# Kernel optimization log

Hardware: AMD Instinct MI355X
Metric: run time of the kernel (lower is better)

The kernel has to match this reference:

```python
import jax, jax.numpy as jnp
import numpy as np

K = 16        # neighbors (init kwarg k)
LN_EPS = 1e-5


def setup_inputs() -> dict:
    key = jax.random.key(0)
    ks = jax.random.split(key, 12)
    B, N, C, H = 4, 4096, 64, 12
    w = lambda k, s: jax.random.normal(k, s, jnp.float32) * 0.05
    d = {}
    d["x"] = jax.random.normal(ks[0], (B, N, C), jnp.float32)
    d["pos"] = jax.random.uniform(ks[1], (B, N, 3), jnp.float32)
    # to_q / to_k / to_v (bias=False). Stored as [in,out]; apply as x @ W.
    d["Wq"] = w(ks[2], (C, C)); d["Wk"] = w(ks[3], (C, C)); d["Wv"] = w(ks[4], (C, C))
    # pos_mlp: Linear(3,H) -> LayerNorm(H) -> ReLU -> Linear(H,C)
    d["p_w1"] = w(ks[5], (3, H)); d["p_b1"] = jnp.zeros((H,), jnp.float32)
    d["p_g"] = jnp.ones((H,), jnp.float32); d["p_be"] = jnp.zeros((H,), jnp.float32)
    d["p_w2"] = w(ks[6], (H, C)); d["p_b2"] = jnp.zeros((C,), jnp.float32)
    # attn_mlp: Linear(C,C) -> LayerNorm(C) -> ReLU -> Linear(C,C)
    d["a_w1"] = w(ks[7], (C, C)); d["a_b1"] = jnp.zeros((C,), jnp.float32)
    d["a_g"] = jnp.ones((C,), jnp.float32); d["a_be"] = jnp.zeros((C,), jnp.float32)
    d["a_w2"] = w(ks[8], (C, C)); d["a_b2"] = jnp.zeros((C,), jnp.float32)
    return d


def _ln(x, g, b):
    m = x.mean(-1, keepdims=True)
    v = ((x - m) ** 2).mean(-1, keepdims=True)
    return (x - m) * jax.lax.rsqrt(v + LN_EPS) * g + b


def _gather(feats, idx):
    # feats [B,N,C], idx [B,N,K] -> [B,N,K,C]
    return jax.vmap(lambda f, i: f[i])(feats, idx)


def reference(x, pos, Wq, Wk, Wv, p_w1, p_b1, p_g, p_be, p_w2, p_b2,
              a_w1, a_b1, a_g, a_be, a_w2, a_b2):
    # knn_points(pos, pos, K, return_sorted=True): K nearest by squared dist
    sq = jnp.sum(pos * pos, axis=-1)                       # [B,N]
    d2 = sq[:, :, None] + sq[:, None, :] - 2.0 * jnp.einsum('bnd,bmd->bnm', pos, pos)
    _, idx = jax.lax.top_k(-d2, K)                         # [B,N,K], ascending distance
    knn_xyz = _gather(pos, idx)                            # [B,N,K,3]
    q = x @ Wq                                             # [B,N,C]
    k = _gather(x @ Wk, idx)                               # [B,N,K,C]
    v = _gather(x @ Wv, idx)                               # [B,N,K,C]
    rel = pos[:, :, None, :] - knn_xyz                     # [B,N,K,3]
    pos_enc = jax.nn.relu(_ln(rel @ p_w1 + p_b1, p_g, p_be)) @ p_w2 + p_b2   # [B,N,K,C]
    w_in = q[:, :, None, :] - k + pos_enc                  # [B,N,K,C]
    attn = jax.nn.relu(_ln(w_in @ a_w1 + a_b1, a_g, a_be)) @ a_w2 + a_b2
    attn = jax.nn.softmax(attn, axis=-2)                   # softmax over K neighbors
    return jnp.einsum('bikd,bikd->bid', attn, v + pos_enc) # [B,N,C]
```

## Files before the change

kernel.cpp:

```cpp
#include <hip/hip_runtime.h>
#include <math.h>

#define NPTS 4096
#define KNN 16
#define LN_EPS 1e-5f

#define BOOT 128
#define CAP0 32
#define TRIG 24
#define CAP1 72
#define C1S  928
#define CHSZ 1056
#define SEG  352


__global__ __launch_bounds__(256) void proj3_kernel(
    const float* __restrict__ x, const float* __restrict__ Wq,
    const float* __restrict__ Wk, const float* __restrict__ Wv,
    float* __restrict__ qf, float* __restrict__ kf, float* __restrict__ vf) {
  int g = blockIdx.x * 256 + threadIdx.x;
  int r = g >> 6, c = g & 63;
  float sq = 0.f, sk = 0.f, sv = 0.f;
  for (int i = 0; i < 64; ++i) {
    float xv = x[r*64 + i];
    sq += xv * Wq[i*64 + c];
    sk += xv * Wk[i*64 + c];
    sv += xv * Wv[i*64 + c];
  }
  qf[g] = sq; kf[g] = sk; vf[g] = sv;
}

__global__ __launch_bounds__(256) void wtrans_kernel(
    const float* __restrict__ a_w1, const float* __restrict__ a_w2,
    float* __restrict__ w1t, float* __restrict__ w2t) {
  int e = blockIdx.x * 256 + threadIdx.x;
  int i = e >> 6, c = e & 63;
  w1t[c*64 + i] = a_w1[e];
  w2t[c*64 + i] = a_w2[e];
}

#define INSERT_CHAIN(DD, JJ)                                          \
  do {                                                                \
    float dd = (DD); int jj = (JJ);                                   \
    _Pragma("unroll")                                                 \
    for (int v = 0; v < 16; ++v) {                                    \
      bool sw = dd < ld[v];                                           \
      float nd = sw ? dd : ld[v]; float td = sw ? ld[v] : dd;         \
      int   nj = sw ? jj : lj[v]; int   tj = sw ? lj[v] : jj;         \
      ld[v] = nd; lj[v] = nj; dd = td; jj = tj;                       \
    }                                                                 \
  } while (0)

#define REPLAY0()                                                     \
  do {                                                                \
    for (int i = 0; ; ++i) {                                          \
      unsigned long long alive = __ballot(i < cnt);                   \
      if (!alive) break;                                              \
      if (i < cnt) {                                                  \
        float dd0 = s_buf0[i*128 + bo];                               \
        int   jj0 = __float_as_int(s_buf0[i*128 + bo + 1]);           \
        if (dd0 < ld[15]) INSERT_CHAIN(dd0, jj0);                     \
      }                                                               \
    }                                                                 \
    cnt = 0; thr = ld[15]; s_thr[tid] = thr;                          \
  } while (0)

#define GROUP_D2(SBASE)                                               \
  float4 p[8];                                                        \
  _Pragma("unroll")                                                   \
  for (int u = 0; u < 8; ++u) p[u] = s_p[(SBASE) + u];                \
  float d2v[8];                                                       \
  _Pragma("unroll")                                                   \
  for (int u = 0; u < 8; ++u) {                                       \
    float acc = __fmul_rn(qx, p[u].x);                                \
    acc = __fmaf_rn(qy, p[u].y, acc);                                 \
    acc = __fmaf_rn(qz, p[u].z, acc);                                 \
    d2v[u] = __fsub_rn(__fadd_rn(sqn, p[u].w), __fmul_rn(2.0f, acc)); \
  }

#define TREE_OFFS(THRV)                                               \
  int f0 = (d2v[0] < (THRV)) ? 1 : 0, f1 = (d2v[1] < (THRV)) ? 1 : 0, \
      f2 = (d2v[2] < (THRV)) ? 1 : 0, f3 = (d2v[3] < (THRV)) ? 1 : 0, \
      f4 = (d2v[4] < (THRV)) ? 1 : 0, f5 = (d2v[5] < (THRV)) ? 1 : 0, \
      f6 = (d2v[6] < (THRV)) ? 1 : 0, f7 = (d2v[7] < (THRV)) ? 1 : 0; \
  int s01 = f0+f1, s23 = f2+f3, s45 = f4+f5, s67 = f6+f7;             \
  int s03 = s01+s23, s47 = s45+s67;                                   \
  int o[8];                                                           \
  o[0] = cnt;        o[1] = cnt + f0;   o[2] = cnt + s01;             \
  o[3] = cnt + s01 + f2;                o[4] = cnt + s03;             \
  o[5] = o[4] + f4;  o[6] = o[4] + s45; o[7] = o[6] + f6;

__global__ __launch_bounds__(256) void knn_gated4_kernel(
    const float* __restrict__ pos, int* __restrict__ idx_out) {
  __shared__ __align__(16) float4 s_p[NPTS];
  __shared__ __align__(16) float  s_buf0[CAP0*128];
  __shared__ int   s_j1[3][(CAP1+1)*64];
  __shared__ float s_thr[64];
  __shared__ int   s_cnt1[3][64];
  __shared__ int   s_gen;
  __shared__ int   s_ovf;

  int t = threadIdx.x;
  int tid = t & 63, w = t >> 6, b = blockIdx.y;
  const float* pb = pos + b*NPTS*3;
  for (int j = t; j < NPTS; j += 256) {
    float px = pb[j*3+0], py = pb[j*3+1], pz = pb[j*3+2];
    float sq = __fadd_rn(__fadd_rn(__fmul_rn(px,px), __fmul_rn(py,py)),
                         __fmul_rn(pz,pz));
    s_p[j] = make_float4(px, py, pz, sq);
  }
  if (t < 64) s_thr[t] = INFINITY;
  if (t == 0) { s_ovf = 0; s_gen = 0; }
  __syncthreads();

  int n = blockIdx.x * 64 + tid;
  float4 qp = s_p[n];
  float qx = qp.x, qy = qp.y, qz = qp.z, sqn = qp.w;
  float ld[16]; int lj[16];
#pragma unroll
  for (int u = 0; u < 16; ++u) { ld[u] = INFINITY; lj[u] = 0x7fffffff; }

  for (int s = 0; s < BOOT; s += 8) {
    GROUP_D2(s)
#pragma unroll
    for (int u = 0; u < 8; ++u) {
      float d2 = d2v[u];
      if (d2 < ld[15]) INSERT_CHAIN(d2, s + u);
    }
  }
  float thr = ld[15];
  int bo = tid << 1;
  int cnt = 0;

  if (w == 0) {
    for (int s = BOOT; s < C1S; s += 8) {
      GROUP_D2(s)
      TREE_OFFS(thr)
#pragma unroll
      for (int u = 0; u < 8; ++u) {
        s_buf0[o[u]*128 + bo]     = d2v[u];
        s_buf0[o[u]*128 + bo + 1] = __int_as_float(s + u);
      }
      cnt += s03 + s47;
      int done = s + 8;
      bool pub = ((done & 127) == 0) && done >= 256 && done <= 896;
      if (pub || __ballot(cnt >= TRIG) != 0ULL) {
        REPLAY0();
        if (pub) {
          __threadfence_block();
          s_gen = (done >> 7) - 1;
        }
      }
    }
    REPLAY0();
    __syncthreads();

    int ovf = s_ovf;
    for (int ch = 0; ch < 3; ++ch) {
      int cs = C1S + ch*CHSZ;
      if (ovf & (1 << ch)) {
        int ce = cs + CHSZ;
        for (int s = cs; s < ce; s += 8) {
          GROUP_D2(s)
          TREE_OFFS(thr)
#pragma unroll
          for (int u = 0; u < 8; ++u) {
            s_buf0[o[u]*128 + bo]     = d2v[u];
            s_buf0[o[u]*128 + bo + 1] = __int_as_float(s + u);
          }
          cnt += s03 + s47;
          if (__ballot(cnt >= TRIG) != 0ULL) REPLAY0();
        }
        REPLAY0();
      } else {
        const int* jb = &s_j1[ch][0];
        int cc = s_cnt1[ch][tid];
        int jn = (0 < cc) ? jb[tid] : 0;
        float4 pn = s_p[jn];
        for (int i = 0; ; ++i) {
          unsigned long long alive = __ballot(i < cc);
          if (!alive) break;
          int jj0 = jn; float4 pj = pn;
          int ix = i + 1;
          jn = (ix < cc) ? jb[ix*64 + tid] : 0;
          pn = s_p[jn];
          if (i < cc) {
            float acc = __fmul_rn(qx, pj.x);
            acc = __fmaf_rn(qy, pj.y, acc);
            acc = __fmaf_rn(qz, pj.z, acc);
            float dd0 = __fsub_rn(__fadd_rn(sqn, pj.w), __fmul_rn(2.0f, acc));
            if (dd0 < ld[15]) INSERT_CHAIN(dd0, jj0);
          }
        }
      }
    }
    int* outp = idx_out + (b*NPTS + n)*KNN;
#pragma unroll
    for (int u = 0; u < 16; ++u) outp[u] = b*NPTS + lj[u];
  } else {
    int cs = C1S + (w-1)*CHSZ;
    int* jb = &s_j1[w-1][0];
    float thrW = thr;
#pragma unroll
    for (int seg = 0; seg < 3; ++seg) {
      int need = 2*seg + 2;
      while (*((volatile int*)&s_gen) < need) __builtin_amdgcn_s_sleep(2);
      thrW = fminf(thrW, *((volatile float*)&s_thr[tid]));
      int ss = cs + seg*SEG, se = ss + SEG;
      for (int s = ss; s < se; s += 8) {
        GROUP_D2(s)
        TREE_OFFS(thrW)
#pragma unroll
        for (int u = 0; u < 8; ++u) {
          int oc = (o[u] <= CAP1) ? o[u] : CAP1;
          jb[oc*64 + tid] = s + u;
        }
        cnt += s03 + s47;
      }
    }
    s_cnt1[w-1][tid] = (cnt <= CAP1) ? cnt : CAP1;
    if (cnt > CAP1) atomicOr(&s_ovf, 1 << (w-1));
    __syncthreads();
  }
}

__device__ __forceinline__ float wsum64(float v) {
  v += __shfl_xor(v, 1);
  v += __shfl_xor(v, 2);
  v += __shfl_xor(v, 4);
  v += __shfl_xor(v, 8);
  v += __shfl_xor(v, 16);
  v += __shfl_xor(v, 32);
  return v;
}

__device__ __forceinline__ float bcast(float v, int lane) {
  return __int_as_float(__builtin_amdgcn_readlane(__float_as_int(v), lane));
}

__global__ __launch_bounds__(256, 6) void fuse_kernel(
    const float* __restrict__ pos, const int* __restrict__ idx,
    const float* __restrict__ qf, const float* __restrict__ kf,
    const float* __restrict__ vf,
    const float* __restrict__ p_w1, const float* __restrict__ p_b1,
    const float* __restrict__ p_g, const float* __restrict__ p_be,
    const float* __restrict__ p_w2, const float* __restrict__ p_b2,
    const float* __restrict__ w1t, const float* __restrict__ a_b1,
    const float* __restrict__ a_g, const float* __restrict__ a_be,
    const float* __restrict__ w2t, const float* __restrict__ a_b2,
    float* __restrict__ out) {
  __shared__ int   s_j[16];
  __shared__ float s_h[16][12];
  __shared__ __align__(16) float s_ve[16][64];
  __shared__ __align__(16) float s_t2[16][64];
  __shared__ float s_pw2[768];

  int tid = threadIdx.x;
  int p = blockIdx.x;
  int c = tid & 63, kq = tid >> 6;

  for (int e = tid; e < 768; e += 256) s_pw2[e] = p_w2[e];

  if (tid < 16) {
    int j = idx[p*KNN + tid];
    s_j[tid] = j;
    float rx = pos[p*3+0] - pos[j*3+0];
    float ry = pos[p*3+1] - pos[j*3+1];
    float rz = pos[p*3+2] - pos[j*3+2];
    float hv[12];
    float mean = 0.f;
#pragma unroll
    for (int h = 0; h < 12; ++h) {
      float v = rx*p_w1[h] + ry*p_w1[12+h] + rz*p_w1[24+h] + p_b1[h];
      hv[h] = v; mean += v;
    }
    mean *= (1.0f/12.0f);
    float var = 0.f;
#pragma unroll
    for (int h = 0; h < 12; ++h) { float d = hv[h] - mean; var += d*d; }
    var *= (1.0f/12.0f);
    float rs = rsqrtf(var + LN_EPS);
#pragma unroll
    for (int h = 0; h < 12; ++h) {
      float a = (hv[h] - mean)*rs*p_g[h] + p_be[h];
      s_h[tid][h] = fmaxf(a, 0.f);
    }
  }
  __syncthreads();

  float win0, win1, win2, win3;
  {
    float qv = qf[p*64 + c];
    float pb2 = p_b2[c];
    float pe0 = pb2, pe1 = pb2, pe2 = pb2, pe3 = pb2;
#pragma unroll
    for (int h = 0; h < 12; ++h) {
      float wv = s_pw2[h*64 + c];
      pe0 = __fmaf_rn(s_h[kq][h],    wv, pe0);
      pe1 = __fmaf_rn(s_h[4+kq][h],  wv, pe1);
      pe2 = __fmaf_rn(s_h[8+kq][h],  wv, pe2);
      pe3 = __fmaf_rn(s_h[12+kq][h], wv, pe3);
    }
    int j0 = s_j[kq], j1 = s_j[4+kq], j2 = s_j[8+kq], j3 = s_j[12+kq];
    win0 = qv - kf[j0*64 + c] + pe0;  s_ve[kq][c]    = vf[j0*64 + c] + pe0;
    win1 = qv - kf[j1*64 + c] + pe1;  s_ve[4+kq][c]  = vf[j1*64 + c] + pe1;
    win2 = qv - kf[j2*64 + c] + pe2;  s_ve[8+kq][c]  = vf[j2*64 + c] + pe2;
    win3 = qv - kf[j3*64 + c] + pe3;  s_ve[12+kq][c] = vf[j3*64 + c] + pe3;
  }

  const float* w1c = w1t + c*64;
  float ab1 = a_b1[c];
  float a0 = ab1, a1 = ab1, a2 = ab1, a3 = ab1;
#pragma unroll
  for (int ii = 0; ii < 16; ++ii) {
    float4 wa = *(const float4*)(w1c + 4*ii);
#pragma unroll
    for (int q = 0; q < 4; ++q) {
      int i = 4*ii + q;
      float wv = (q == 0) ? wa.x : (q == 1) ? wa.y : (q == 2) ? wa.z : wa.w;
      float b0 = bcast(win0, i), b1 = bcast(win1, i);
      float b2 = bcast(win2, i), b3 = bcast(win3, i);
      a0 = __fmaf_rn(b0, wv, a0);
      a1 = __fmaf_rn(b1, wv, a1);
      a2 = __fmaf_rn(b2, wv, a2);
      a3 = __fmaf_rn(b3, wv, a3);
    }
  }

  float ag = a_g[c], abe = a_be[c];
  float r0, r1, r2, r3;
  {
    float m = wsum64(a0) * (1.0f/64.0f); float d = a0 - m;
    float var = wsum64(d*d) * (1.0f/64.0f);
    r0 = fmaxf(d*rsqrtf(var + LN_EPS)*ag + abe, 0.f);
  }
  {
    float m = wsum64(a1) * (1.0f/64.0f); float d = a1 - m;
    float var = wsum64(d*d) * (1.0f/64.0f);
    r1 = fmaxf(d*rsqrtf(var + LN_EPS)*ag + abe, 0.f);
  }
  {
    float m = wsum64(a2) * (1.0f/64.0f); float d = a2 - m;
    float var = wsum64(d*d) * (1.0f/64.0f);
    r2 = fmaxf(d*rsqrtf(var + LN_EPS)*ag + abe, 0.f);
  }
  {
    float m = wsum64(a3) * (1.0f/64.0f); float d = a3 - m;
    float var = wsum64(d*d) * (1.0f/64.0f);
    r3 = fmaxf(d*rsqrtf(var + LN_EPS)*ag + abe, 0.f);
  }

  const float* w2c = w2t + c*64;
  float ab2 = a_b2[c];
  float t0 = ab2, t1 = ab2, t2 = ab2, t3 = ab2;
#pragma unroll
  for (int ii = 0; ii < 16; ++ii) {
    float4 wa = *(const float4*)(w2c + 4*ii);
#pragma unroll
    for (int q = 0; q < 4; ++q) {
      int i = 4*ii + q;
      float wv = (q == 0) ? wa.x : (q == 1) ? wa.y : (q == 2) ? wa.z : wa.w;
      float b0 = bcast(r0, i), b1 = bcast(r1, i);
      float b2 = bcast(r2, i), b3 = bcast(r3, i);
      t0 = __fmaf_rn(b0, wv, t0);
      t1 = __fmaf_rn(b1, wv, t1);
      t2 = __fmaf_rn(b2, wv, t2);
      t3 = __fmaf_rn(b3, wv, t3);
    }
  }
  s_t2[kq][c]    = t0;
  s_t2[4+kq][c]  = t1;
  s_t2[8+kq][c]  = t2;
  s_t2[12+kq][c] = t3;
  __syncthreads();

  if (tid < 64) {
    float mx = -INFINITY;
    for (int k = 0; k < 16; ++k) mx = fmaxf(mx, s_t2[k][tid]);
    float se = 0.f, po = 0.f;
    for (int k = 0; k < 16; ++k) {
      float e = expf(s_t2[k][tid] - mx);
      se += e; po += e * s_ve[k][tid];
    }
    out[p*64 + tid] = po / se;
  }
}

extern "C" void kernel_launch(void* const* d_in, const int* in_sizes, int n_in,
                              void* d_out, int out_size, void* d_ws, size_t ws_size,
                              hipStream_t stream) {
  const float* x    = (const float*)d_in[0];
  const float* pos  = (const float*)d_in[1];
  const float* Wq   = (const float*)d_in[2];
  const float* Wk   = (const float*)d_in[3];
  const float* Wv   = (const float*)d_in[4];
  const float* p_w1 = (const float*)d_in[5];
  const float* p_b1 = (const float*)d_in[6];
  const float* p_g  = (const float*)d_in[7];
  const float* p_be = (const float*)d_in[8];
  const float* p_w2 = (const float*)d_in[9];
  const float* p_b2 = (const float*)d_in[10];
  const float* a_w1 = (const float*)d_in[11];
  const float* a_b1 = (const float*)d_in[12];
  const float* a_g  = (const float*)d_in[13];
  const float* a_be = (const float*)d_in[14];
  const float* a_w2 = (const float*)d_in[15];
  const float* a_b2 = (const float*)d_in[16];

  float* ws   = (float*)d_ws;
  float* qf   = ws;
  float* kf   = qf + 1048576;
  float* vf   = kf + 1048576;
  int*   idx  = (int*)(vf + 1048576);
  float* w1t  = (float*)(idx + 262144);
  float* w2t  = w1t + 4096;
  float* outp = (float*)d_out;

  hipLaunchKernelGGL(wtrans_kernel, dim3(16), dim3(256), 0, stream,
                     a_w1, a_w2, w1t, w2t);
  hipLaunchKernelGGL(proj3_kernel, dim3(4096), dim3(256), 0, stream,
                     x, Wq, Wk, Wv, qf, kf, vf);
  hipLaunchKernelGGL(knn_gated4_kernel, dim3(64, 4), dim3(256), 0, stream,
                     pos, idx);
  hipLaunchKernelGGL(fuse_kernel, dim3(16384), dim3(256), 0, stream,
                     pos, idx, qf, kf, vf,
                     p_w1, p_b1, p_g, p_be, p_w2, p_b2,
                     w1t, a_b1, a_g, a_be, w2t, a_b2, outp);
}
```

Measured before the change: 529.5 us.

## Double-buffer KNN point loads and stage attention MLP weights in LDS

New measurement: 460.4 us. 1.15x faster.

```diff
diff --git a/kernel.cpp b/kernel.cpp
--- a/kernel.cpp
+++ b/kernel.cpp
@@ -30,15 +30,6 @@
   qf[g] = sq; kf[g] = sk; vf[g] = sv;
 }
 
-__global__ __launch_bounds__(256) void wtrans_kernel(
-    const float* __restrict__ a_w1, const float* __restrict__ a_w2,
-    float* __restrict__ w1t, float* __restrict__ w2t) {
-  int e = blockIdx.x * 256 + threadIdx.x;
-  int i = e >> 6, c = e & 63;
-  w1t[c*64 + i] = a_w1[e];
-  w2t[c*64 + i] = a_w2[e];
-}
-
 #define INSERT_CHAIN(DD, JJ)                                          \
   do {                                                                \
     float dd = (DD); int jj = (JJ);                                   \
@@ -65,18 +56,21 @@
     cnt = 0; thr = ld[15]; s_thr[tid] = thr;                          \
   } while (0)
 
-#define GROUP_D2(SBASE)                                               \
-  float4 p[8];                                                        \
+#define LOADP(P, SBASE)                                               \
   _Pragma("unroll")                                                   \
-  for (int u = 0; u < 8; ++u) p[u] = s_p[(SBASE) + u];                \
+  for (int u = 0; u < 8; ++u) P[u] = s_p[(SBASE) + u];
+
+#define D2V(P)                                                        \
   float d2v[8];                                                       \
   _Pragma("unroll")                                                   \
   for (int u = 0; u < 8; ++u) {                                       \
-    float acc = __fmul_rn(qx, p[u].x);                                \
-    acc = __fmaf_rn(qy, p[u].y, acc);                                 \
-    acc = __fmaf_rn(qz, p[u].z, acc);                                 \
-    d2v[u] = __fsub_rn(__fadd_rn(sqn, p[u].w), __fmul_rn(2.0f, acc)); \
-  }
+    float acc = __fmul_rn(qx, P[u].x);                                \
+    acc = __fmaf_rn(qy, P[u].y, acc);                                 \
+    acc = __fmaf_rn(qz, P[u].z, acc);                                 \
+    d2v[u] = __fsub_rn(__fadd_rn(sqn, P[u].w), __fmul_rn(2.0f, acc)); \
+  }
+
+#define GROUP_D2(SBASE) float4 p[8]; LOADP(p, SBASE) D2V(p)
 
 #define TREE_OFFS(THRV)                                               \
   int f0 = (d2v[0] < (THRV)) ? 1 : 0, f1 = (d2v[1] < (THRV)) ? 1 : 0, \
@@ -90,6 +84,46 @@
   o[3] = cnt + s01 + f2;                o[4] = cnt + s03;             \
   o[5] = o[4] + f4;  o[6] = o[4] + s45; o[7] = o[6] + f6;
 
+#define PROC_BOOT(P, S) {                                             \
+    D2V(P)                                                            \
+    _Pragma("unroll")                                                 \
+    for (int u = 0; u < 8; ++u) {                                     \
+      float d2 = d2v[u];                                              \
+      if (d2 < ld[15]) INSERT_CHAIN(d2, (S) + u);                     \
+    }                                                                 \
+  }
+
+#define PROC_W0(P, S) {                                               \
+    D2V(P)                                                            \
+    TREE_OFFS(thr)                                                    \
+    _Pragma("unroll")                                                 \
+    for (int u = 0; u < 8; ++u) {                                     \
+      s_buf0[o[u]*128 + bo]     = d2v[u];                             \
+      s_buf0[o[u]*128 + bo + 1] = __int_as_float((S) + u);            \
+    }                                                                 \
+    cnt += s03 + s47;                                                 \
+    int done = (S) + 8;                                               \
+    bool pub = ((done & 127) == 0) && done >= 256 && done <= 896;     \
+    if (pub || __ballot(cnt >= TRIG) != 0ULL) {                       \
+      REPLAY0();                                                      \
+      if (pub) {                                                      \
+        __threadfence_block();                                        \
+        s_gen = (done >> 7) - 1;                                      \
+      }                                                               \
+    }                                                                 \
+  }
+
+#define PROC_W13(P, S) {                                              \
+    D2V(P)                                                            \
+    TREE_OFFS(thrW)                                                   \
+    _Pragma("unroll")                                                 \
+    for (int u = 0; u < 8; ++u) {                                     \
+      int oc = (o[u] <= CAP1) ? o[u] : CAP1;                          \
+      jb[oc*64 + tid] = (S) + u;                                      \
+    }                                                                 \
+    cnt += s03 + s47;                                                 \
+  }
+
 __global__ __launch_bounds__(256) void knn_gated4_kernel(
     const float* __restrict__ pos, int* __restrict__ idx_out) {
   __shared__ __align__(16) float4 s_p[NPTS];
@@ -120,37 +154,25 @@
 #pragma unroll
   for (int u = 0; u < 16; ++u) { ld[u] = INFINITY; lj[u] = 0x7fffffff; }
 
-  for (int s = 0; s < BOOT; s += 8) {
-    GROUP_D2(s)
-#pragma unroll
-    for (int u = 0; u < 8; ++u) {
-      float d2 = d2v[u];
-      if (d2 < ld[15]) INSERT_CHAIN(d2, s + u);
-    }
+  float4 pA[8], pB[8];
+
+  LOADP(pA, 0)
+  for (int s = 0; s < BOOT; s += 16) {
+    LOADP(pB, s + 8)
+    PROC_BOOT(pA, s)
+    LOADP(pA, s + 16)
+    PROC_BOOT(pB, s + 8)
   }
   float thr = ld[15];
   int bo = tid << 1;
   int cnt = 0;
 
   if (w == 0) {
-    for (int s = BOOT; s < C1S; s += 8) {
-      GROUP_D2(s)
-      TREE_OFFS(thr)
-#pragma unroll
-      for (int u = 0; u < 8; ++u) {
-        s_buf0[o[u]*128 + bo]     = d2v[u];
-        s_buf0[o[u]*128 + bo + 1] = __int_as_float(s + u);
-      }
-      cnt += s03 + s47;
-      int done = s + 8;
-      bool pub = ((done & 127) == 0) && done >= 256 && done <= 896;
-      if (pub || __ballot(cnt >= TRIG) != 0ULL) {
-        REPLAY0();
-        if (pub) {
-          __threadfence_block();
-          s_gen = (done >> 7) - 1;
-        }
-      }
+    for (int s = BOOT; s < C1S; s += 16) {
+      LOADP(pB, s + 8)
+      PROC_W0(pA, s)
+      LOADP(pA, s + 16)
+      PROC_W0(pB, s + 8)
     }
     REPLAY0();
     __syncthreads();
@@ -201,21 +223,19 @@
     int cs = C1S + (w-1)*CHSZ;
     int* jb = &s_j1[w-1][0];
     float thrW = thr;
-#pragma unroll
+#pragma unroll 1
     for (int seg = 0; seg < 3; ++seg) {
       int need = 2*seg + 2;
       while (*((volatile int*)&s_gen) < need) __builtin_amdgcn_s_sleep(2);
       thrW = fminf(thrW, *((volatile float*)&s_thr[tid]));
       int ss = cs + seg*SEG, se = ss + SEG;
-      for (int s = ss; s < se; s += 8) {
-        GROUP_D2(s)
-        TREE_OFFS(thrW)
-#pragma unroll
-        for (int u = 0; u < 8; ++u) {
-          int oc = (o[u] <= CAP1) ? o[u] : CAP1;
-          jb[oc*64 + tid] = s + u;
-        }
-        cnt += s03 + s47;
+      LOADP(pA, ss)
+      for (int s = ss; s < se; s += 16) {
+        LOADP(pB, s + 8)
+        PROC_W13(pA, s)
+        int sn = s + 16; if (sn >= se) sn = ss;
+        LOADP(pA, sn)
+        PROC_W13(pB, s + 8)
       }
     }
     s_cnt1[w-1][tid] = (cnt <= CAP1) ? cnt : CAP1;
@@ -238,27 +258,30 @@
   return __int_as_float(__builtin_amdgcn_readlane(__float_as_int(v), lane));
 }
 
-__global__ __launch_bounds__(256, 6) void fuse_kernel(
+__global__ __launch_bounds__(256) void fuse_kernel(
     const float* __restrict__ pos, const int* __restrict__ idx,
     const float* __restrict__ qf, const float* __restrict__ kf,
     const float* __restrict__ vf,
     const float* __restrict__ p_w1, const float* __restrict__ p_b1,
     const float* __restrict__ p_g, const float* __restrict__ p_be,
     const float* __restrict__ p_w2, const float* __restrict__ p_b2,
-    const float* __restrict__ w1t, const float* __restrict__ a_b1,
+    const float* __restrict__ a_w1, const float* __restrict__ a_b1,
     const float* __restrict__ a_g, const float* __restrict__ a_be,
-    const float* __restrict__ w2t, const float* __restrict__ a_b2,
+    const float* __restrict__ a_w2, const float* __restrict__ a_b2,
     float* __restrict__ out) {
   __shared__ int   s_j[16];
   __shared__ float s_h[16][12];
   __shared__ __align__(16) float s_ve[16][64];
   __shared__ __align__(16) float s_t2[16][64];
   __shared__ float s_pw2[768];
+  __shared__ float s_w1[4096];
+  __shared__ float s_w2[4096];
 
   int tid = threadIdx.x;
   int p = blockIdx.x;
   int c = tid & 63, kq = tid >> 6;
 
+  for (int e = tid; e < 4096; e += 256) { s_w1[e] = a_w1[e]; s_w2[e] = a_w2[e]; }
   for (int e = tid; e < 768; e += 256) s_pw2[e] = p_w2[e];
 
   if (tid < 16) {
@@ -308,23 +331,17 @@
     win3 = qv - kf[j3*64 + c] + pe3;  s_ve[12+kq][c] = vf[j3*64 + c] + pe3;
   }
 
-  const float* w1c = w1t + c*64;
   float ab1 = a_b1[c];
   float a0 = ab1, a1 = ab1, a2 = ab1, a3 = ab1;
 #pragma unroll
-  for (int ii = 0; ii < 16; ++ii) {
-    float4 wa = *(const float4*)(w1c + 4*ii);
-#pragma unroll
-    for (int q = 0; q < 4; ++q) {
-      int i = 4*ii + q;
-      float wv = (q == 0) ? wa.x : (q == 1) ? wa.y : (q == 2) ? wa.z : wa.w;
-      float b0 = bcast(win0, i), b1 = bcast(win1, i);
-      float b2 = bcast(win2, i), b3 = bcast(win3, i);
-      a0 = __fmaf_rn(b0, wv, a0);
-      a1 = __fmaf_rn(b1, wv, a1);
-      a2 = __fmaf_rn(b2, wv, a2);
-      a3 = __fmaf_rn(b3, wv, a3);
-    }
+  for (int i = 0; i < 64; ++i) {
+    float wv = s_w1[i*64 + c];
+    float b0 = bcast(win0, i), b1 = bcast(win1, i);
+    float b2 = bcast(win2, i), b3 = bcast(win3, i);
+    a0 = __fmaf_rn(b0, wv, a0);
+    a1 = __fmaf_rn(b1, wv, a1);
+    a2 = __fmaf_rn(b2, wv, a2);
+    a3 = __fmaf_rn(b3, wv, a3);
   }
 
   float ag = a_g[c], abe = a_be[c];
@@ -350,23 +367,17 @@
     r3 = fmaxf(d*rsqrtf(var + LN_EPS)*ag + abe, 0.f);
   }
 
-  const float* w2c = w2t + c*64;
   float ab2 = a_b2[c];
   float t0 = ab2, t1 = ab2, t2 = ab2, t3 = ab2;
 #pragma unroll
-  for (int ii = 0; ii < 16; ++ii) {
-    float4 wa = *(const float4*)(w2c + 4*ii);
-#pragma unroll
-    for (int q = 0; q < 4; ++q) {
-      int i = 4*ii + q;
-      float wv = (q == 0) ? wa.x : (q == 1) ? wa.y : (q == 2) ? wa.z : wa.w;
-      float b0 = bcast(r0, i), b1 = bcast(r1, i);
-      float b2 = bcast(r2, i), b3 = bcast(r3, i);
-      t0 = __fmaf_rn(b0, wv, t0);
-      t1 = __fmaf_rn(b1, wv, t1);
-      t2 = __fmaf_rn(b2, wv, t2);
-      t3 = __fmaf_rn(b3, wv, t3);
-    }
+  for (int i = 0; i < 64; ++i) {
+    float wv = s_w2[i*64 + c];
+    float b0 = bcast(r0, i), b1 = bcast(r1, i);
+    float b2 = bcast(r2, i), b3 = bcast(r3, i);
+    t0 = __fmaf_rn(b0, wv, t0);
+    t1 = __fmaf_rn(b1, wv, t1);
+    t2 = __fmaf_rn(b2, wv, t2);
+    t3 = __fmaf_rn(b3, wv, t3);
   }
   s_t2[kq][c]    = t0;
   s_t2[4+kq][c]  = t1;
@@ -412,12 +423,8 @@
   float* kf   = qf + 1048576;
   float* vf   = kf + 1048576;
   int*   idx  = (int*)(vf + 1048576);
-  float* w1t  = (float*)(idx + 262144);
-  float* w2t  = w1t + 4096;
   float* outp = (float*)d_out;
 
-  hipLaunchKernelGGL(wtrans_kernel, dim3(16), dim3(256), 0, stream,
-                     a_w1, a_w2, w1t, w2t);
   hipLaunchKernelGGL(proj3_kernel, dim3(4096), dim3(256), 0, stream,
                      x, Wq, Wk, Wv, qf, kf, vf);
   hipLaunchKernelGGL(knn_gated4_kernel, dim3(64, 4), dim3(256), 0, stream,
@@ -425,5 +432,5 @@
   hipLaunchKernelGGL(fuse_kernel, dim3(16384), dim3(256), 0, stream,
                      pos, idx, qf, kf, vf,
                      p_w1, p_b1, p_g, p_be, p_w2, p_b2,
-                     w1t, a_b1, a_g, a_be, w2t, a_b2, outp);
-}
+                     a_w1, a_b1, a_g, a_be, a_w2, a_b2, outp);
+}
```
